# Optimization experiments

Measured on AMD Instinct MI355X. Metric: run time of the kernel, lower is better.

The kernel has to match this reference:

```python
import jax, jax.numpy as jnp
import numpy as np

B, SQ, SK = 2, 2048, 2048
D_MODEL, N_HEADS = 1024, 16
D_HEAD = D_MODEL // N_HEADS
LN_EPS = 1e-5


def _ln(x, w, b):
    # per-head LayerNorm over last dim (d_head)
    mu = jnp.mean(x, axis=-1, keepdims=True)
    var = jnp.mean(jnp.square(x - mu), axis=-1, keepdims=True)
    return (x - mu) * jax.lax.rsqrt(var + LN_EPS) * w + b


def setup_inputs() -> dict:
    key = jax.random.key(0)
    ks = jax.random.split(key, 8)
    sd = 1.0 / np.sqrt(D_MODEL)
    so = 1.0 / np.sqrt(D_HEAD)
    return {
        "x_q": jax.random.normal(ks[0], (B, SQ, D_MODEL), jnp.float32),
        "x_kv": jax.random.normal(ks[1], (B, SK, D_MODEL), jnp.float32),
        "mask": jnp.tril(jnp.ones((SQ, SK), dtype=bool)),  # causal
        "W_Q": jax.random.normal(ks[2], (N_HEADS, D_MODEL, D_HEAD), jnp.float32) * sd,
        "W_K": jax.random.normal(ks[3], (N_HEADS, D_MODEL, D_HEAD), jnp.float32) * sd,
        "W_V": jax.random.normal(ks[4], (N_HEADS, D_MODEL, D_HEAD), jnp.float32) * sd,
        "W_O": jax.random.normal(ks[5], (N_HEADS, D_HEAD, D_MODEL), jnp.float32) * so,
        "b_Q": jnp.zeros((N_HEADS, D_HEAD), jnp.float32),
        "b_K": jnp.zeros((N_HEADS, D_HEAD), jnp.float32),
        "b_V": jnp.zeros((N_HEADS, D_HEAD), jnp.float32),
        "b_O": jnp.zeros((D_MODEL,), jnp.float32),
        "ln1_w": jnp.ones((D_HEAD,), jnp.float32),
        "ln1_b": jnp.zeros((D_HEAD,), jnp.float32),
        "ln2_w": jnp.ones((D_HEAD,), jnp.float32),
        "ln2_b": jnp.zeros((D_HEAD,), jnp.float32),
    }


def reference(x_q, x_kv, mask, W_Q, W_K, W_V, W_O, b_Q, b_K, b_V, b_O,
              ln1_w, ln1_b, ln2_w, ln2_b):
    # QKV projections: b s d, n d h -> b s n h
    q = jnp.einsum('bsd,ndh->bsnh', x_q, W_Q) + b_Q
    k = jnp.einsum('bsd,ndh->bsnh', x_kv, W_K) + b_K
    v = jnp.einsum('bsd,ndh->bsnh', x_kv, W_V) + b_V
    # QK-norm (ln_first=False, rope=None -> just apply LN after projections)
    q = _ln(q, ln1_w, ln1_b)
    k = _ln(k, ln2_w, ln2_b)
    # NOTE: no 1/sqrt(d_head) scaling, matching the original module
    att = jnp.einsum('bqnh,bknh->bnqk', q, k)
    att = jnp.where(mask, att, -jnp.inf)
    probas = jax.nn.softmax(att, axis=-1)
    z = jnp.einsum('bnqk,bknh->bqnh', probas, v)
    out = jnp.einsum('bqnh,nhd->bqd', z, W_O) + b_O
    return (out, k, v)
```

## Files before the change

kernel.cpp:

```cpp
#include <hip/hip_runtime.h>
#include <hip/hip_bf16.h>

#define B_   2
#define SQ_  2048
#define DM_  1024
#define NH_  16
#define DH_  64

typedef __attribute__((ext_vector_type(8))) short          bf16x8;
typedef __attribute__((ext_vector_type(8))) unsigned short u16x8;
typedef __attribute__((ext_vector_type(4))) float          f32x4;

__device__ __forceinline__ unsigned short f2bf(float f) {
    union { __hip_bfloat16 h; unsigned short u; } c;
    c.h = __float2bfloat16(f);
    return c.u;
}
__device__ __forceinline__ float gsum16(float v) {
    v += __shfl_xor(v, 1);
    v += __shfl_xor(v, 2);
    v += __shfl_xor(v, 4);
    v += __shfl_xor(v, 8);
    return v;
}

__device__ __forceinline__ void gll16(const unsigned short* g, unsigned short* l) {
    __builtin_amdgcn_global_load_lds(
        (const __attribute__((address_space(1))) unsigned int*)g,
        (__attribute__((address_space(3))) unsigned int*)l,
        16, 0, 0);
}

__global__ __launch_bounds__(256) void prep_all(
    const float* __restrict__ W_Q, const float* __restrict__ W_K,
    const float* __restrict__ W_V, const float* __restrict__ W_O,
    const float* __restrict__ x_q, const float* __restrict__ x_kv,
    unsigned short* __restrict__ WTq, unsigned short* __restrict__ WTkv,
    unsigned short* __restrict__ WTo,
    unsigned short* __restrict__ xqbf, unsigned short* __restrict__ xkvbf)
{
    const int bid = blockIdx.x, tid = threadIdx.x;
    if (bid >= 1024) {
        const int cid = bid - 1024;
        const float* src = (cid < 256) ? x_q : x_kv;
        unsigned short* dst = (cid < 256) ? xqbf : xkvbf;
        const size_t base = (size_t)(cid & 255) * 16384 + tid * 4;
#pragma unroll
        for (int i = 0; i < 16; ++i) {
            const float4 v = *(const float4*)(src + base + i * 1024);
            ushort4 o;
            o.x = f2bf(v.x); o.y = f2bf(v.y); o.z = f2bf(v.z); o.w = f2bf(v.w);
            *(ushort4*)(dst + base + i * 1024) = o;
        }
        return;
    }
    __shared__ float t[64][65];
    const float* src; unsigned short* dst; int R, C, r0, c0;
    if (bid < 768) {
        const int which = bid >> 8, rem = bid & 255;
        const int rblk = rem & 15, zz = rem >> 4;
        src = (which == 0) ? W_Q : (which == 1) ? W_K : W_V;
        dst = (which == 0) ? WTq : (which == 1) ? WTkv : (WTkv + (1u << 20));
        src += (size_t)65536 * zz;
        dst += (size_t)65536 * zz;
        R = 1024; C = 64; r0 = rblk * 64; c0 = 0;
    } else {
        const int rem = bid - 768;
        src = W_O; dst = WTo; R = 1024; C = 1024;
        r0 = (rem & 15) * 64; c0 = (rem >> 4) * 64;
    }
    const int lr = tid >> 6, lc = tid & 63;
#pragma unroll
    for (int i = 0; i < 16; ++i)
        t[lr + i * 4][lc] = src[(size_t)(r0 + lr + i * 4) * C + c0 + lc];
    __syncthreads();
    const int u = tid & 15, w0 = tid >> 4;
#pragma unroll
    for (int i = 0; i < 4; ++i) {
        const int cl = w0 + i * 16;
        ushort4 o;
        o.x = f2bf(t[4 * u + 0][cl]);
        o.y = f2bf(t[4 * u + 1][cl]);
        o.z = f2bf(t[4 * u + 2][cl]);
        o.w = f2bf(t[4 * u + 3][cl]);
        *(ushort4*)&dst[(size_t)(c0 + cl) * R + r0 + 4 * u] = o;
    }
}

template <int TM, int MODE>
__device__ __forceinline__ void gemm_body(
    unsigned short (*__restrict__ As)[64], unsigned short (*__restrict__ Bs)[64],
    int bx, int by, const unsigned short* __restrict__ Abf,
    const unsigned short* __restrict__ WT,
    const float* __restrict__ biasK, const float* __restrict__ biasV,
    const float* __restrict__ lnw, const float* __restrict__ lnb,
    float* __restrict__ Cf, float* __restrict__ Cf2,
    unsigned short* __restrict__ Cb, unsigned short* __restrict__ CbT, int tid)
{
    constexpr int MI = TM / 32;
    constexpr int AJ = TM / 32;

    const int m0 = by * TM;
    const int c0 = bx * 128;

    const int wid = tid >> 6, lane = tid & 63;
    const int wm = (wid >> 1) * (TM / 2);
    const int wn = (wid & 1) * 64;
    const int l15 = lane & 15, qd = lane >> 4;

    const int srow  = tid >> 3;
    const int pslot = tid & 7;
    const int sslot = pslot ^ (srow & 7);
    const unsigned short* Ag = Abf + (size_t)(m0 + srow) * 1024 + sslot * 8;
    const unsigned short* Bg = WT  + (size_t)(c0 + srow) * 1024 + sslot * 8;
    unsigned short* Al = &As[srow][pslot * 8];
    unsigned short* Bl = &Bs[srow][pslot * 8];

    const f32x4 zero4 = {0.f, 0.f, 0.f, 0.f};
    f32x4 acc[MI][4];
#pragma unroll
    for (int mi = 0; mi < MI; ++mi)
#pragma unroll
        for (int ni = 0; ni < 4; ++ni) acc[mi][ni] = zero4;

    const int r7 = l15 & 7;

    for (int kb = 0; kb < 16; ++kb) {
        const size_t kof = (size_t)kb * 64;
        __syncthreads();
#pragma unroll
        for (int j = 0; j < AJ; ++j)
            gll16(Ag + (size_t)j * 32 * 1024 + kof, Al + j * 32 * 64);
#pragma unroll
        for (int j = 0; j < 4; ++j)
            gll16(Bg + (size_t)j * 32 * 1024 + kof, Bl + j * 32 * 64);
        __syncthreads();
#pragma unroll
        for (int ks = 0; ks < 2; ++ks) {
            const int cs = ((ks * 4 + qd) ^ r7) * 8;
            bf16x8 af[MI], bfr[4];
#pragma unroll
            for (int mi = 0; mi < MI; ++mi)
                af[mi] = *(const bf16x8*)&As[wm + mi * 16 + l15][cs];
#pragma unroll
            for (int ni = 0; ni < 4; ++ni)
                bfr[ni] = *(const bf16x8*)&Bs[wn + ni * 16 + l15][cs];
#pragma unroll
            for (int mi = 0; mi < MI; ++mi)
#pragma unroll
                for (int ni = 0; ni < 4; ++ni)
                    acc[mi][ni] = __builtin_amdgcn_mfma_f32_16x16x32_bf16(
                        af[mi], bfr[ni], acc[mi][ni], 0, 0, 0);
        }
    }

    const float* bias = (MODE == 1 && c0 >= 1024) ? biasV : biasK;
    float bv[4];
#pragma unroll
    for (int ni = 0; ni < 4; ++ni) bv[ni] = bias[(c0 + wn + ni * 16 + l15) & 1023];
#pragma unroll
    for (int mi = 0; mi < MI; ++mi)
#pragma unroll
        for (int ni = 0; ni < 4; ++ni)
#pragma unroll
            for (int r = 0; r < 4; ++r) acc[mi][ni][r] += bv[ni];

    if constexpr (MODE != 2) {
        const bool doLN = (MODE == 0) || (c0 < 1024);
        if (doLN) {
            float w4[4], lb4[4];
#pragma unroll
            for (int ni = 0; ni < 4; ++ni) {
                w4[ni]  = lnw[ni * 16 + l15];
                lb4[ni] = lnb[ni * 16 + l15];
            }
#pragma unroll
            for (int mi = 0; mi < MI; ++mi)
#pragma unroll
                for (int r = 0; r < 4; ++r) {
                    float s1 = acc[mi][0][r] + acc[mi][1][r] + acc[mi][2][r] + acc[mi][3][r];
                    const float mu = gsum16(s1) * (1.0f / 64.0f);
                    float s2 = acc[mi][0][r] * acc[mi][0][r] + acc[mi][1][r] * acc[mi][1][r]
                             + acc[mi][2][r] * acc[mi][2][r] + acc[mi][3][r] * acc[mi][3][r];
                    const float var = gsum16(s2) * (1.0f / 64.0f) - mu * mu;
                    const float rstd = rsqrtf(var + 1e-5f);
#pragma unroll
                    for (int ni = 0; ni < 4; ++ni)
                        acc[mi][ni][r] = (acc[mi][ni][r] - mu) * rstd * w4[ni] + lb4[ni];
                }
        }
    }

    if constexpr (MODE == 0) {
#pragma unroll
        for (int mi = 0; mi < MI; ++mi)
#pragma unroll
            for (int r = 0; r < 4; ++r) {
                const size_t grow = m0 + wm + mi * 16 + qd * 4 + r;
#pragma unroll
                for (int ni = 0; ni < 4; ++ni)
                    Cb[grow * 1024 + c0 + wn + ni * 16 + l15] = f2bf(acc[mi][ni][r]);
            }
    } else if constexpr (MODE == 2) {
#pragma unroll
        for (int mi = 0; mi < MI; ++mi)
#pragma unroll
            for (int r = 0; r < 4; ++r) {
                const size_t grow = m0 + wm + mi * 16 + qd * 4 + r;
#pragma unroll
                for (int ni = 0; ni < 4; ++ni)
                    Cf[grow * 1024 + c0 + wn + ni * 16 + l15] = acc[mi][ni][r];
            }
    } else {
        if (c0 < 1024) {
#pragma unroll
            for (int mi = 0; mi < MI; ++mi)
#pragma unroll
                for (int r = 0; r < 4; ++r) {
                    const size_t grow = m0 + wm + mi * 16 + qd * 4 + r;
#pragma unroll
                    for (int ni = 0; ni < 4; ++ni) {
                        const int gcol = c0 + wn + ni * 16 + l15;
                        Cf[grow * 1024 + gcol] = acc[mi][ni][r];
                        Cb[grow * 1024 + gcol] = f2bf(acc[mi][ni][r]);
                    }
                }
        } else {
#pragma unroll
            for (int mi = 0; mi < MI; ++mi) {
                const int growb = m0 + wm + mi * 16 + qd * 4;
                const int bb_ = growb >> 11, ss = growb & 2047;
#pragma unroll
                for (int ni = 0; ni < 4; ++ni) {
                    const int gv = c0 - 1024 + wn + ni * 16 + l15;
                    const int hh = gv >> 6, dd = gv & 63;
#pragma unroll
                    for (int r = 0; r < 4; ++r)
                        Cf2[(size_t)(growb + r) * 1024 + gv] = acc[mi][ni][r];
                    ushort4 w;
                    w.x = f2bf(acc[mi][ni][0]); w.y = f2bf(acc[mi][ni][1]);
                    w.z = f2bf(acc[mi][ni][2]); w.w = f2bf(acc[mi][ni][3]);
                    *(ushort4*)&CbT[(((size_t)bb_ * NH_ + hh) * DH_ + dd) * SQ_ + ss] = w;
                }
            }
        }
    }
}

__global__ __launch_bounds__(256) void qkv_fused(
    const unsigned short* __restrict__ xqbf, const unsigned short* __restrict__ xkvbf,
    const unsigned short* __restrict__ WTq, const unsigned short* __restrict__ WTkv,
    const float* __restrict__ b_Q, const float* __restrict__ b_K,
    const float* __restrict__ b_V,
    const float* __restrict__ ln1w, const float* __restrict__ ln1b,
    const float* __restrict__ ln2w, const float* __restrict__ ln2b,
    float* __restrict__ kout, float* __restrict__ vout,
    unsigned short* __restrict__ qz, unsigned short* __restrict__ kbf,
    unsigned short* __restrict__ vbfT)
{
    __shared__ __align__(16) unsigned short As[64][64];
    __shared__ __align__(16) unsigned short Bs[128][64];
    const int bid = blockIdx.x, tid = threadIdx.x;
    if (bid < 1024) {
        gemm_body<64, 1>(As, Bs, bid & 15, bid >> 4, xkvbf, WTkv, b_K, b_V,
                         ln2w, ln2b, kout, vout, kbf, vbfT, tid);
    } else {
        const int b2 = bid - 1024;
        gemm_body<64, 0>(As, Bs, b2 & 7, b2 >> 3, xqbf, WTq, b_Q, nullptr,
                         ln1w, ln1b, nullptr, nullptr, qz, nullptr, tid);
    }
}

__global__ __launch_bounds__(256) void o_gemm(
    const unsigned short* __restrict__ zbf, const unsigned short* __restrict__ WTo,
    const float* __restrict__ b_O, float* __restrict__ out)
{
    __shared__ __align__(16) unsigned short As[64][64];
    __shared__ __align__(16) unsigned short Bs[128][64];
    gemm_body<64, 2>(As, Bs, blockIdx.x, blockIdx.y, zbf, WTo, b_O, nullptr,
                     nullptr, nullptr, out, nullptr, nullptr, nullptr, threadIdx.x);
}

__global__ __launch_bounds__(256) void attn_mfma(
    unsigned short* __restrict__ qz, const unsigned short* __restrict__ kbf,
    const unsigned short* __restrict__ vbfT)
{
    __shared__ __align__(16) unsigned short Ks[2][64][72];
    __shared__ __align__(16) unsigned short VsT[2][64][72];
    __shared__ __align__(16) unsigned short Ps[64][72];

    const int tid = threadIdx.x;
    const int h = blockIdx.y, b = blockIdx.z;
    const int wid = tid >> 6, lane = tid & 63;
    const int l15 = lane & 15, qd = lane >> 4;
    const int srow = tid >> 2, scol = (tid & 3) * 16;

    const size_t kbase = (size_t)b * SQ_ * DM_ + (size_t)h * DH_;
    const size_t vbase = ((size_t)b * NH_ + h) * DH_ * (size_t)SQ_;
    const f32x4 zero4 = {0.f, 0.f, 0.f, 0.f};
    const float LOG2E = 1.44269504f, MBIAS = 46.1662413f;

    for (int pass = 0; pass < 2; ++pass) {
        const int qt = pass ? blockIdx.x : 31 - blockIdx.x;

        bf16x8 qf[2];
        {
            const unsigned short* qp =
                qz + kbase + (size_t)(qt * 64 + wid * 16 + l15) * DM_ + qd * 8;
            qf[0] = *(const bf16x8*)(qp);
            qf[1] = *(const bf16x8*)(qp + 32);
        }

        f32x4 z[4];
#pragma unroll
        for (int ni = 0; ni < 4; ++ni) z[ni] = zero4;
        float l_i = 0.f;

        {
            const unsigned short* ks = kbf + kbase + (size_t)srow * DM_ + scol;
            const u16x8 a0 = *(const u16x8*)(ks);
            const u16x8 a1 = *(const u16x8*)(ks + 8);
            const unsigned short* vs = vbfT + vbase + (size_t)srow * SQ_ + scol;
            const u16x8 b0 = *(const u16x8*)(vs);
            const u16x8 b1 = *(const u16x8*)(vs + 8);
            *(u16x8*)&Ks[0][srow][scol + 0]  = a0;
            *(u16x8*)&Ks[0][srow][scol + 8]  = a1;
            *(u16x8*)&VsT[0][srow][scol + 0] = b0;
            *(u16x8*)&VsT[0][srow][scol + 8] = b1;
        }
        __syncthreads();

        for (int kt = 0; kt <= qt; ++kt) {
            const int cur = kt & 1;

            u16x8 kr0, kr1, vr0, vr1;
            if (kt < qt) {
                const unsigned short* ks =
                    kbf + kbase + (size_t)((kt + 1) * 64 + srow) * DM_ + scol;
                kr0 = *(const u16x8*)(ks);
                kr1 = *(const u16x8*)(ks + 8);
                const unsigned short* vs =
                    vbfT + vbase + (size_t)srow * SQ_ + (kt + 1) * 64 + scol;
                vr0 = *(const u16x8*)(vs);
                vr1 = *(const u16x8*)(vs + 8);
            }

            f32x4 s[4];
#pragma unroll
            for (int mi = 0; mi < 4; ++mi) s[mi] = zero4;
#pragma unroll
            for (int ks2 = 0; ks2 < 2; ++ks2)
#pragma unroll
                for (int mi = 0; mi < 4; ++mi) {
                    const bf16x8 af =
                        *(const bf16x8*)&Ks[cur][mi * 16 + l15][ks2 * 32 + qd * 8];
                    s[mi] = __builtin_amdgcn_mfma_f32_16x16x32_bf16(af, qf[ks2], s[mi], 0, 0, 0);
                }

            if (kt == qt) {
#pragma unroll
                for (int mi = 0; mi < 4; ++mi)
#pragma unroll
                    for (int r = 0; r < 4; ++r)
                        if (mi * 16 + qd * 4 + r > wid * 16 + l15) s[mi][r] = -3.0e38f;
            }

            float ts[4];
#pragma unroll
            for (int mi = 0; mi < 4; ++mi) {
#pragma unroll
                for (int r = 0; r < 4; ++r)
                    s[mi][r] = __builtin_amdgcn_exp2f(fmaf(s[mi][r], LOG2E, -MBIAS));
                ts[mi] = (s[mi][0] + s[mi][1]) + (s[mi][2] + s[mi][3]);
            }
            float rs = (ts[0] + ts[1]) + (ts[2] + ts[3]);
            rs += __shfl_xor(rs, 16);
            rs += __shfl_xor(rs, 32);
            l_i += rs;

#pragma unroll
            for (int mi = 0; mi < 4; ++mi) {
                ushort4 w;
                w.x = f2bf(s[mi][0]); w.y = f2bf(s[mi][1]);
                w.z = f2bf(s[mi][2]); w.w = f2bf(s[mi][3]);
                *(ushort4*)&Ps[wid * 16 + l15][mi * 16 + qd * 4] = w;
            }

#pragma unroll
            for (int ks2 = 0; ks2 < 2; ++ks2) {
                const bf16x8 ap = *(const bf16x8*)&Ps[wid * 16 + l15][ks2 * 32 + qd * 8];
#pragma unroll
                for (int ni = 0; ni < 4; ++ni) {
                    const bf16x8 bv =
                        *(const bf16x8*)&VsT[cur][ni * 16 + l15][ks2 * 32 + qd * 8];
                    z[ni] = __builtin_amdgcn_mfma_f32_16x16x32_bf16(ap, bv, z[ni], 0, 0, 0);
                }
            }

            if (kt < qt) {
                *(u16x8*)&Ks[cur ^ 1][srow][scol + 0]  = kr0;
                *(u16x8*)&Ks[cur ^ 1][srow][scol + 8]  = kr1;
                *(u16x8*)&VsT[cur ^ 1][srow][scol + 0] = vr0;
                *(u16x8*)&VsT[cur ^ 1][srow][scol + 8] = vr1;
            }
            __syncthreads();
        }

        const float linv = 1.0f / l_i;
#pragma unroll
        for (int r = 0; r < 4; ++r) {
            const float lr_ = __shfl(linv, qd * 4 + r);
            const size_t row = (size_t)qt * 64 + wid * 16 + qd * 4 + r;
#pragma unroll
            for (int ni = 0; ni < 4; ++ni)
                qz[kbase + row * DM_ + ni * 16 + l15] = f2bf(z[ni][r] * lr_);
        }
    }
}

extern "C" void kernel_launch(void* const* d_in, const int* in_sizes, int n_in,
                              void* d_out, int out_size, void* d_ws, size_t ws_size,
                              hipStream_t stream)
{
    const float* x_q  = (const float*)d_in[0];
    const float* x_kv = (const float*)d_in[1];
    const float* W_Q  = (const float*)d_in[3];
    const float* W_K  = (const float*)d_in[4];
    const float* W_V  = (const float*)d_in[5];
    const float* W_O  = (const float*)d_in[6];
    const float* b_Q  = (const float*)d_in[7];
    const float* b_K  = (const float*)d_in[8];
    const float* b_V  = (const float*)d_in[9];
    const float* b_O  = (const float*)d_in[10];
    const float* ln1w = (const float*)d_in[11];
    const float* ln1b = (const float*)d_in[12];
    const float* ln2w = (const float*)d_in[13];
    const float* ln2b = (const float*)d_in[14];

    const size_t NTOK = (size_t)B_ * SQ_;
    float* out  = (float*)d_out;
    float* kout = out + NTOK * DM_;
    float* vout = kout + NTOK * DM_;

    unsigned short* xqbf  = (unsigned short*)out;
    unsigned short* xkvbf = xqbf + (1u << 22);

    unsigned short* wsu  = (unsigned short*)d_ws;
    unsigned short* WTq  = wsu;
    unsigned short* WTkv = WTq + (1u << 20);
    unsigned short* WTo  = WTkv + (2u << 20);
    unsigned short* qz   = WTo + (1u << 20);
    unsigned short* kbf  = qz + (1u << 22);
    unsigned short* vbfT = kbf + (1u << 22);

    prep_all<<<1536, 256, 0, stream>>>(W_Q, W_K, W_V, W_O, x_q, x_kv,
                                       WTq, WTkv, WTo, xqbf, xkvbf);

    qkv_fused<<<1536, 256, 0, stream>>>(xqbf, xkvbf, WTq, WTkv, b_Q, b_K, b_V,
                                        ln1w, ln1b, ln2w, ln2b,
                                        kout, vout, qz, kbf, vbfT);

    attn_mfma<<<dim3(16, NH_, B_), 256, 0, stream>>>(qz, kbf, vbfT);

    o_gemm<<<dim3(8, 64), 256, 0, stream>>>(qz, WTo, b_O, out);
}
```

Baseline: 231.7 us.

## Keep P in registers for PV MFMA, shrink O-GEMM tile, widen prep grid

The attention kernel no longer round-trips the softmax probabilities through shared memory. It packs them directly into bf16x4 register fragments and feeds them to the 16x16x16 bf16 MFMA, removing the LDS stores and reloads for P. The output GEMM uses 32-row M tiles to double the block count. The input-conversion part of prep_all runs on twice as many blocks with half the work each. The tradeoffs are twice as many smaller MFMA instructions in the PV product and more redundant weight loads in the O GEMM.

```diff
diff --git a/kernel.cpp b/kernel.cpp
--- a/kernel.cpp
+++ b/kernel.cpp
@@ -8,6 +8,7 @@
 #define DH_  64
 
 typedef __attribute__((ext_vector_type(8))) short          bf16x8;
+typedef __attribute__((ext_vector_type(4))) short          bf16x4;
 typedef __attribute__((ext_vector_type(8))) unsigned short u16x8;
 typedef __attribute__((ext_vector_type(4))) float          f32x4;
 
@@ -22,6 +23,15 @@
     v += __shfl_xor(v, 4);
     v += __shfl_xor(v, 8);
     return v;
+}
+
+__device__ __forceinline__ f32x4 mfma16(bf16x4 a, bf16x4 b, f32x4 c) {
+#if __has_builtin(__builtin_amdgcn_mfma_f32_16x16x16bf16_1k)
+    return __builtin_amdgcn_mfma_f32_16x16x16bf16_1k(a, b, c, 0, 0, 0);
+#else
+    asm("v_mfma_f32_16x16x16_bf16 %0, %1, %2, %0" : "+v"(c) : "v"(a), "v"(b));
+    return c;
+#endif
 }
 
 __device__ __forceinline__ void gll16(const unsigned short* g, unsigned short* l) {
@@ -42,11 +52,11 @@
     const int bid = blockIdx.x, tid = threadIdx.x;
     if (bid >= 1024) {
         const int cid = bid - 1024;
-        const float* src = (cid < 256) ? x_q : x_kv;
-        unsigned short* dst = (cid < 256) ? xqbf : xkvbf;
-        const size_t base = (size_t)(cid & 255) * 16384 + tid * 4;
-#pragma unroll
-        for (int i = 0; i < 16; ++i) {
+        const float* src = (cid < 512) ? x_q : x_kv;
+        unsigned short* dst = (cid < 512) ? xqbf : xkvbf;
+        const size_t base = (size_t)(cid & 511) * 8192 + tid * 4;
+#pragma unroll
+        for (int i = 0; i < 8; ++i) {
             const float4 v = *(const float4*)(src + base + i * 1024);
             ushort4 o;
             o.x = f2bf(v.x); o.y = f2bf(v.y); o.z = f2bf(v.z); o.w = f2bf(v.w);
@@ -97,7 +107,7 @@
     float* __restrict__ Cf, float* __restrict__ Cf2,
     unsigned short* __restrict__ Cb, unsigned short* __restrict__ CbT, int tid)
 {
-    constexpr int MI = TM / 32;
+    constexpr int MI = (TM >= 32) ? TM / 32 : 1;
     constexpr int AJ = TM / 32;
 
     const int m0 = by * TM;
@@ -111,10 +121,11 @@
     const int srow  = tid >> 3;
     const int pslot = tid & 7;
     const int sslot = pslot ^ (srow & 7);
-    const unsigned short* Ag = Abf + (size_t)(m0 + srow) * 1024 + sslot * 8;
+    const unsigned short* Ag = Abf + (size_t)(m0 + (srow % TM)) * 1024 + sslot * 8;
     const unsigned short* Bg = WT  + (size_t)(c0 + srow) * 1024 + sslot * 8;
-    unsigned short* Al = &As[srow][pslot * 8];
+    unsigned short* Al = &As[srow % TM][pslot * 8];
     unsigned short* Bl = &Bs[srow][pslot * 8];
+    const bool athr = (srow < TM);
 
     const f32x4 zero4 = {0.f, 0.f, 0.f, 0.f};
     f32x4 acc[MI][4];
@@ -128,9 +139,13 @@
     for (int kb = 0; kb < 16; ++kb) {
         const size_t kof = (size_t)kb * 64;
         __syncthreads();
-#pragma unroll
-        for (int j = 0; j < AJ; ++j)
-            gll16(Ag + (size_t)j * 32 * 1024 + kof, Al + j * 32 * 64);
+        if (TM >= 64) {
+#pragma unroll
+            for (int j = 0; j < AJ; ++j)
+                gll16(Ag + (size_t)j * 32 * 1024 + kof, Al + j * 32 * 64);
+        } else if (athr) {
+            gll16(Ag + kof, Al);
+        }
 #pragma unroll
         for (int j = 0; j < 4; ++j)
             gll16(Bg + (size_t)j * 32 * 1024 + kof, Bl + j * 32 * 64);
@@ -275,9 +290,9 @@
     const unsigned short* __restrict__ zbf, const unsigned short* __restrict__ WTo,
     const float* __restrict__ b_O, float* __restrict__ out)
 {
-    __shared__ __align__(16) unsigned short As[64][64];
+    __shared__ __align__(16) unsigned short As[32][64];
     __shared__ __align__(16) unsigned short Bs[128][64];
-    gemm_body<64, 2>(As, Bs, blockIdx.x, blockIdx.y, zbf, WTo, b_O, nullptr,
+    gemm_body<32, 2>(As, Bs, blockIdx.x, blockIdx.y, zbf, WTo, b_O, nullptr,
                      nullptr, nullptr, out, nullptr, nullptr, nullptr, threadIdx.x);
 }
 
@@ -287,7 +302,6 @@
 {
     __shared__ __align__(16) unsigned short Ks[2][64][72];
     __shared__ __align__(16) unsigned short VsT[2][64][72];
-    __shared__ __align__(16) unsigned short Ps[64][72];
 
     const int tid = threadIdx.x;
     const int h = blockIdx.y, b = blockIdx.z;
@@ -366,12 +380,17 @@
             }
 
             float ts[4];
+            bf16x4 pa[4];
 #pragma unroll
             for (int mi = 0; mi < 4; ++mi) {
 #pragma unroll
                 for (int r = 0; r < 4; ++r)
                     s[mi][r] = __builtin_amdgcn_exp2f(fmaf(s[mi][r], LOG2E, -MBIAS));
                 ts[mi] = (s[mi][0] + s[mi][1]) + (s[mi][2] + s[mi][3]);
+                pa[mi][0] = (short)f2bf(s[mi][0]);
+                pa[mi][1] = (short)f2bf(s[mi][1]);
+                pa[mi][2] = (short)f2bf(s[mi][2]);
+                pa[mi][3] = (short)f2bf(s[mi][3]);
             }
             float rs = (ts[0] + ts[1]) + (ts[2] + ts[3]);
             rs += __shfl_xor(rs, 16);
@@ -379,23 +398,13 @@
             l_i += rs;
 
 #pragma unroll
-            for (int mi = 0; mi < 4; ++mi) {
-                ushort4 w;
-                w.x = f2bf(s[mi][0]); w.y = f2bf(s[mi][1]);
-                w.z = f2bf(s[mi][2]); w.w = f2bf(s[mi][3]);
-                *(ushort4*)&Ps[wid * 16 + l15][mi * 16 + qd * 4] = w;
-            }
-
-#pragma unroll
-            for (int ks2 = 0; ks2 < 2; ++ks2) {
-                const bf16x8 ap = *(const bf16x8*)&Ps[wid * 16 + l15][ks2 * 32 + qd * 8];
+            for (int mi = 0; mi < 4; ++mi)
 #pragma unroll
                 for (int ni = 0; ni < 4; ++ni) {
-                    const bf16x8 bv =
-                        *(const bf16x8*)&VsT[cur][ni * 16 + l15][ks2 * 32 + qd * 8];
-                    z[ni] = __builtin_amdgcn_mfma_f32_16x16x32_bf16(ap, bv, z[ni], 0, 0, 0);
+                    const bf16x4 bv =
+                        *(const bf16x4*)&VsT[cur][ni * 16 + l15][mi * 16 + qd * 4];
+                    z[ni] = mfma16(pa[mi], bv, z[ni]);
                 }
-            }
 
             if (kt < qt) {
                 *(u16x8*)&Ks[cur ^ 1][srow][scol + 0]  = kr0;
@@ -453,7 +462,7 @@
     unsigned short* kbf  = qz + (1u << 22);
     unsigned short* vbfT = kbf + (1u << 22);
 
-    prep_all<<<1536, 256, 0, stream>>>(W_Q, W_K, W_V, W_O, x_q, x_kv,
+    prep_all<<<2048, 256, 0, stream>>>(W_Q, W_K, W_V, W_O, x_q, x_kv,
                                        WTq, WTkv, WTo, xqbf, xkvbf);
 
     qkv_fused<<<1536, 256, 0, stream>>>(xqbf, xkvbf, WTq, WTkv, b_Q, b_K, b_V,
@@ -462,5 +471,5 @@
 
     attn_mfma<<<dim3(16, NH_, B_), 256, 0, stream>>>(qz, kbf, vbfT);
 
-    o_gemm<<<dim3(8, 64), 256, 0, stream>>>(qz, WTo, b_O, out);
-}
+    o_gemm<<<dim3(8, 128), 256, 0, stream>>>(qz, WTo, b_O, out);
+}
```

Result: no change. 233.1 us (+0.6%).
